# Kernel tuning notes

Hardware: AMD Instinct MI355X
Metric: run time of the kernel (lower is better)

Reference implementation:

```python
import jax, jax.numpy as jnp
import numpy as np

B, S, F, T = 32, 512, 512, 1024  # batch, seq_len(channel dim), feat_dim, time length


def setup_inputs() -> dict:
    key = jax.random.key(0)
    ks = jax.random.split(key, 6)
    scale = 0.05  # keep tanh/softmax in a non-saturated regime
    return {
        "z_robot": jax.random.normal(ks[0], (B, S, T), dtype=jnp.float32),
        "z_human": jax.random.normal(ks[1], (B, S, T), dtype=jnp.float32),
        "W_b": jax.random.normal(ks[2], (S, S), dtype=jnp.float32) * scale,
        "W_q": jax.random.normal(ks[3], (F, S), dtype=jnp.float32) * scale,
        "W_v": jax.random.normal(ks[4], (F, S), dtype=jnp.float32) * scale,
        "w_hq": jax.random.normal(ks[5], (1, F), dtype=jnp.float32) * scale,
    }


def reference(z_robot, z_human, W_b, W_q, W_v, w_hq):
    # aux = W_b @ z_human : [B, S, Th]
    aux = jnp.einsum('su,buh->bsh', W_b, z_human)
    # C = tanh(z_robot^T @ aux) : [B, Tr, Th]
    C = jnp.tanh(jnp.einsum('bst,bsh->bth', z_robot, aux))
    # aux2 = W_v @ z_human : [B, F, Th];  aux3 = W_q @ z_robot : [B, F, Tr]
    aux2 = jnp.einsum('fs,bsh->bfh', W_v, z_human)
    aux3 = jnp.einsum('fs,bst->bft', W_q, z_robot)
    # H_q = tanh(aux3 + aux2 @ C^T) : [B, F, Tr]
    H_q = jnp.tanh(aux3 + jnp.einsum('bfh,bth->bft', aux2, C))
    # a_q = softmax(w_hq @ H_q, axis=2) : [B, 1, Tr]
    a_q = jax.nn.softmax(jnp.einsum('of,bft->bot', w_hq, H_q), axis=2)
    # attn = z_robot @ a_q^T : [B, S, 1]
    attn = jnp.einsum('bst,bot->bso', z_robot, a_q)
    return (attn, a_q, C)
```

## Files before the change

### kernel.cpp

```cpp
#include <hip/hip_runtime.h>
#include <math.h>


using f32x4  = __attribute__((ext_vector_type(4))) float;
using bf16x8 = __attribute__((ext_vector_type(8))) short;

__device__ __forceinline__ ushort f2bf(float x) {
    uint u = __float_as_uint(x);
    return (ushort)((u + 0x7fffu + ((u >> 16) & 1u)) >> 16);
}
__device__ __forceinline__ float bf2f(ushort h) { return __uint_as_float((uint)h << 16); }

__device__ __forceinline__ float fast_tanh(float x) {
    return 1.0f - 2.0f / (__expf(2.0f * x) + 1.0f);
}

__device__ __forceinline__ void gll16(const void* g, void* l) {
    __builtin_amdgcn_global_load_lds(
        (__attribute__((address_space(1))) void*)(void*)g,
        (__attribute__((address_space(3))) void*)l, 16, 0, 0);
}


__global__ __launch_bounds__(256)
void transpose_split_k(const float* __restrict__ in, ushort* __restrict__ hi,
                       ushort* __restrict__ lo, int R, int Cn) {
    __shared__ float tile[32][33];
    const int b = blockIdx.z;
    const float* inb = in + (size_t)b * R * Cn;
    const int c0 = blockIdx.x * 32, r0 = blockIdx.y * 32;
    const int tx = threadIdx.x, ty = threadIdx.y;
    #pragma unroll
    for (int i = 0; i < 32; i += 8)
        tile[ty + i][tx] = inb[(size_t)(r0 + ty + i) * Cn + c0 + tx];
    __syncthreads();
    const size_t ob = (size_t)b * R * Cn;
    #pragma unroll
    for (int i = 0; i < 32; i += 8) {
        const float v = tile[tx][ty + i];
        const ushort h = f2bf(v);
        const size_t o = ob + (size_t)(c0 + ty + i) * R + r0 + tx;
        hi[o] = h;
        lo[o] = f2bf(v - bf2f(h));
    }
}

__global__ __launch_bounds__(256)
void convert_split_k(const float* __restrict__ in, ushort* __restrict__ hi,
                     ushort* __restrict__ lo, int n) {
    const int i = blockIdx.x * 256 + threadIdx.x;
    if (i < n) {
        const float v = in[i];
        const ushort h = f2bf(v);
        hi[i] = h;
        if (lo) lo[i] = f2bf(v - bf2f(h));
    }
}

template <int MODE>
__global__ __launch_bounds__(256)
void gemm_split(const ushort* __restrict__ Ahi, const ushort* __restrict__ Alo,
                long sAb, int ldA,
                const ushort* __restrict__ Bhi, const ushort* __restrict__ Blo,
                long sBb, int ldB, int K,
                ushort* __restrict__ Ohi, ushort* __restrict__ Olo,
                float* __restrict__ Of, ushort* __restrict__ O16,
                int ldO, long sOb) {
    __shared__ __align__(16) ushort lds[16384];
    const int b = blockIdx.z, m0 = blockIdx.y * 128, n0 = blockIdx.x * 128;
    const int t = threadIdx.x, l = t & 63, w = t >> 6, wm = w >> 1, wn = w & 1;

    const int srow = l >> 2;
    const int sch  = ((l & 3) ^ (srow & 3)) * 8;
    const ushort* pAh = Ahi + (long)b * sAb + (long)(m0 + w * 32 + srow) * ldA + sch;
    const ushort* pAl = Alo + (long)b * sAb + (long)(m0 + w * 32 + srow) * ldA + sch;
    const ushort* pBh = Bhi + (long)b * sBb + (long)(n0 + w * 32 + srow) * ldB + sch;
    const ushort* pBl = Blo + (long)b * sBb + (long)(n0 + w * 32 + srow) * ldB + sch;

    const int q = l >> 4;
    int offA[4], offB[4];
    #pragma unroll
    for (int i = 0; i < 4; ++i) {
        const int rA = wm * 64 + i * 16 + (l & 15);
        offA[i] = rA * 32 + (q ^ (rA & 3)) * 8;
        const int rB = wn * 64 + i * 16 + (l & 15);
        offB[i] = rB * 32 + (q ^ (rB & 3)) * 8;
    }

    f32x4 acc[4][4] = {};
    for (int k0 = 0; k0 < K; k0 += 32) {
        #pragma unroll
        for (int tt = 0; tt < 2; ++tt) {
            const int lo_ = (w * 32 + tt * 16) * 32;
            gll16(pAh + (long)(tt * 16) * ldA + k0, lds + lo_);
            gll16(pAl + (long)(tt * 16) * ldA + k0, lds + 4096 + lo_);
            gll16(pBh + (long)(tt * 16) * ldB + k0, lds + 8192 + lo_);
            gll16(pBl + (long)(tt * 16) * ldB + k0, lds + 12288 + lo_);
        }
        __syncthreads();
        bf16x8 ah[4], al4[4], bh[4], bl4[4];
        #pragma unroll
        for (int i = 0; i < 4; ++i) {
            ah[i]  = *(const bf16x8*)&lds[offA[i]];
            al4[i] = *(const bf16x8*)&lds[4096 + offA[i]];
            bh[i]  = *(const bf16x8*)&lds[8192 + offB[i]];
            bl4[i] = *(const bf16x8*)&lds[12288 + offB[i]];
        }
        #pragma unroll
        for (int i = 0; i < 4; ++i)
            #pragma unroll
            for (int j = 0; j < 4; ++j) {
                acc[i][j] = __builtin_amdgcn_mfma_f32_16x16x32_bf16(ah[i],  bh[j],  acc[i][j], 0, 0, 0);
                acc[i][j] = __builtin_amdgcn_mfma_f32_16x16x32_bf16(ah[i],  bl4[j], acc[i][j], 0, 0, 0);
                acc[i][j] = __builtin_amdgcn_mfma_f32_16x16x32_bf16(al4[i], bh[j],  acc[i][j], 0, 0, 0);
            }
        __syncthreads();
    }

    const int cl = l & 15, rl = (l >> 4) * 4;
    #pragma unroll
    for (int i = 0; i < 4; ++i)
        #pragma unroll
        for (int r = 0; r < 4; ++r) {
            const long mg = m0 + wm * 64 + i * 16 + rl + r;
            #pragma unroll
            for (int j = 0; j < 4; ++j) {
                const int ng = n0 + wn * 64 + j * 16 + cl;
                const float v = acc[i][j][r];
                const long o = (long)b * sOb + mg * ldO + ng;
                if (MODE == 0) {
                    const ushort h = f2bf(v);
                    Ohi[o] = h;
                    Olo[o] = f2bf(v - bf2f(h));
                } else {
                    const float tv = fast_tanh(v);
                    Of[o] = tv;
                    O16[o] = f2bf(tv);
                }
            }
        }
}

__device__ __forceinline__ void plain_core(
    const ushort* __restrict__ A, long sAb, int ldA,
    const ushort* __restrict__ B, long sBb, int ldB, int K,
    int b, int m0, int n0, ushort* lds, f32x4 (&acc)[4][4]) {
    const int t = threadIdx.x, l = t & 63, w = t >> 6, wm = w >> 1, wn = w & 1;
    const int srow = l >> 3;
    const int sch  = ((l & 7) ^ (srow & 7)) * 8;
    const ushort* pA = A + (long)b * sAb + (long)(m0 + w * 32 + srow) * ldA + sch;
    const ushort* pB = B + (long)b * sBb + (long)(n0 + w * 32 + srow) * ldB + sch;
    const int q = l >> 4;
    int offA[4], offB[4];
    #pragma unroll
    for (int i = 0; i < 4; ++i) {
        const int rA = wm * 64 + i * 16 + (l & 15);
        offA[i] = rA * 64 + (q ^ (rA & 7)) * 8;
        const int rB = wn * 64 + i * 16 + (l & 15);
        offB[i] = 8192 + rB * 64 + (q ^ (rB & 7)) * 8;
    }
    for (int k0 = 0; k0 < K; k0 += 64) {
        #pragma unroll
        for (int tt = 0; tt < 4; ++tt) {
            gll16(pA + (long)(tt * 8) * ldA + k0, lds + (w * 32 + tt * 8) * 64);
            gll16(pB + (long)(tt * 8) * ldB + k0, lds + 8192 + (w * 32 + tt * 8) * 64);
        }
        __syncthreads();
        #pragma unroll
        for (int s = 0; s < 2; ++s) {
            bf16x8 av[4], bv[4];
            #pragma unroll
            for (int i = 0; i < 4; ++i) {
                av[i] = *(const bf16x8*)&lds[offA[i] ^ (s * 32)];
                bv[i] = *(const bf16x8*)&lds[offB[i] ^ (s * 32)];
            }
            #pragma unroll
            for (int i = 0; i < 4; ++i)
                #pragma unroll
                for (int j = 0; j < 4; ++j)
                    acc[i][j] = __builtin_amdgcn_mfma_f32_16x16x32_bf16(av[i], bv[j], acc[i][j], 0, 0, 0);
        }
        __syncthreads();
    }
}

__global__ __launch_bounds__(256)
void gemm_plain_store(const ushort* __restrict__ A, long sAb, int ldA,
                      const ushort* __restrict__ B, long sBb, int ldB, int K,
                      ushort* __restrict__ O, long sOb, int ldO) {
    __shared__ __align__(16) ushort lds[16384];
    const int b = blockIdx.z, m0 = blockIdx.y * 128, n0 = blockIdx.x * 128;
    f32x4 acc[4][4] = {};
    plain_core(A, sAb, ldA, B, sBb, ldB, K, b, m0, n0, lds, acc);
    const int t = threadIdx.x, l = t & 63, w = t >> 6, wm = w >> 1, wn = w & 1;
    const int cl = l & 15, rl = (l >> 4) * 4;
    #pragma unroll
    for (int i = 0; i < 4; ++i)
        #pragma unroll
        for (int r = 0; r < 4; ++r) {
            const long mg = m0 + wm * 64 + i * 16 + rl + r;
            #pragma unroll
            for (int j = 0; j < 4; ++j)
                O[(long)b * sOb + mg * ldO + n0 + wn * 64 + j * 16 + cl] = f2bf(acc[i][j][r]);
        }
}

__global__ __launch_bounds__(256)
void gemm_fused_logits(const ushort* __restrict__ Wq16, const ushort* __restrict__ zrT,
                       const ushort* __restrict__ aux2, const ushort* __restrict__ C16,
                       const float* __restrict__ whq, float* __restrict__ logits) {
    __shared__ __align__(16) ushort lds[16384];
    const int b = blockIdx.z, m0 = blockIdx.y * 128, n0 = blockIdx.x * 128;
    f32x4 acc[4][4] = {};
    plain_core(Wq16, 0, 512, zrT, 524288, 512, 512, b, m0, n0, lds, acc);
    plain_core(aux2, 524288, 1024, C16, 1048576, 1024, 1024, b, m0, n0, lds, acc);
    const int t = threadIdx.x, l = t & 63, w = t >> 6, wm = w >> 1, wn = w & 1;
    float p[4] = {0.f, 0.f, 0.f, 0.f};
    #pragma unroll
    for (int i = 0; i < 4; ++i)
        #pragma unroll
        for (int r = 0; r < 4; ++r) {
            const float wv = whq[m0 + wm * 64 + i * 16 + (l >> 4) * 4 + r];
            #pragma unroll
            for (int j = 0; j < 4; ++j)
                p[j] += wv * fast_tanh(acc[i][j][r]);
        }
    #pragma unroll
    for (int j = 0; j < 4; ++j) {
        p[j] += __shfl_xor(p[j], 16);
        p[j] += __shfl_xor(p[j], 32);
    }
    float* red = (float*)lds;
    __syncthreads();
    if (l < 16) {
        #pragma unroll
        for (int j = 0; j < 4; ++j)
            red[wm * 128 + wn * 64 + j * 16 + l] = p[j];
    }
    __syncthreads();
    if (t < 128)
        atomicAdd(&logits[(long)b * 1024 + n0 + t], red[t] + red[128 + t]);
}

__global__ __launch_bounds__(256)
void softmax_kernel(const float* __restrict__ logits, float* __restrict__ aq, int T) {
    __shared__ float sm[256];
    const int b = blockIdx.x, tid = threadIdx.x;
    float v[4];
    float mx = -1e30f;
    #pragma unroll
    for (int i = 0; i < 4; ++i) {
        v[i] = logits[(size_t)b * T + tid + 256 * i];
        mx = fmaxf(mx, v[i]);
    }
    sm[tid] = mx; __syncthreads();
    for (int s = 128; s > 0; s >>= 1) {
        if (tid < s) sm[tid] = fmaxf(sm[tid], sm[tid + s]);
        __syncthreads();
    }
    mx = sm[0]; __syncthreads();
    float e[4], sum = 0.f;
    #pragma unroll
    for (int i = 0; i < 4; ++i) { e[i] = __expf(v[i] - mx); sum += e[i]; }
    sm[tid] = sum; __syncthreads();
    for (int s = 128; s > 0; s >>= 1) {
        if (tid < s) sm[tid] += sm[tid + s];
        __syncthreads();
    }
    const float inv = 1.0f / sm[0];
    #pragma unroll
    for (int i = 0; i < 4; ++i)
        aq[(size_t)b * T + tid + 256 * i] = e[i] * inv;
}

__global__ __launch_bounds__(256)
void attn_kernel(const float* __restrict__ ZR, const float* __restrict__ aq,
                 float* __restrict__ out, int S, int T) {
    const int b = blockIdx.y;
    const int s = blockIdx.x * 4 + (threadIdx.x >> 6);
    const int lane = threadIdx.x & 63;
    const float* row = ZR + ((size_t)b * S + s) * T;
    const float* a = aq + (size_t)b * T;
    float sum = 0.f;
    for (int t = lane; t < T; t += 64) sum += row[t] * a[t];
    #pragma unroll
    for (int off = 32; off > 0; off >>= 1) sum += __shfl_down(sum, off, 64);
    if (lane == 0) out[(size_t)b * S + s] = sum;
}

#define BM 64
#define BN 64
#define BK 16
#define PAD 4

__global__ __launch_bounds__(256)
void gemm_nn(const float* __restrict__ A, const float* __restrict__ Bm,
             float* __restrict__ D, int M, int N, int K) {
    __shared__ float As[BK][BM + PAD];
    __shared__ float Bs[BK][BN + PAD];
    const int b = blockIdx.z, m0 = blockIdx.y * BM, n0 = blockIdx.x * BN;
    const int tx = threadIdx.x, ty = threadIdx.y, f = ty * 16 + tx;
    const float* Bb = Bm + (size_t)b * K * N;
    float acc[4][4] = {};
    const int ka = f % 16, ma = f / 16, nb = f % 64, kb = f / 64;
    for (int k0 = 0; k0 < K; k0 += BK) {
        #pragma unroll
        for (int i = 0; i < 4; ++i)
            As[ka][ma + 16 * i] = A[(size_t)(m0 + ma + 16 * i) * K + k0 + ka];
        #pragma unroll
        for (int i = 0; i < 4; ++i)
            Bs[kb + 4 * i][nb] = Bb[(size_t)(k0 + kb + 4 * i) * N + n0 + nb];
        __syncthreads();
        #pragma unroll
        for (int k = 0; k < BK; ++k) {
            float av[4], bv[4];
            *(float4*)av = *(const float4*)&As[k][ty * 4];
            *(float4*)bv = *(const float4*)&Bs[k][tx * 4];
            #pragma unroll
            for (int i = 0; i < 4; ++i)
                #pragma unroll
                for (int j = 0; j < 4; ++j) acc[i][j] += av[i] * bv[j];
        }
        __syncthreads();
    }
    float* Db = D + (size_t)b * M * N;
    #pragma unroll
    for (int i = 0; i < 4; ++i)
        *(float4*)&Db[(size_t)(m0 + ty * 4 + i) * N + n0 + tx * 4] =
            make_float4(acc[i][0], acc[i][1], acc[i][2], acc[i][3]);
}

__global__ __launch_bounds__(256)
void gemm_tn_tanh(const float* __restrict__ ZR, const float* __restrict__ AUX,
                  float* __restrict__ C, int M, int N, int K) {
    __shared__ float As[BK][BM + PAD];
    __shared__ float Bs[BK][BN + PAD];
    const int b = blockIdx.z, m0 = blockIdx.y * BM, n0 = blockIdx.x * BN;
    const int tx = threadIdx.x, ty = threadIdx.y, f = ty * 16 + tx;
    const float* ZRb = ZR + (size_t)b * K * M;
    const float* AUXb = AUX + (size_t)b * K * N;
    float acc[4][4] = {};
    const int nl = f % 64, kl = f / 64;
    for (int k0 = 0; k0 < K; k0 += BK) {
        #pragma unroll
        for (int i = 0; i < 4; ++i)
            As[kl + 4 * i][nl] = ZRb[(size_t)(k0 + kl + 4 * i) * M + m0 + nl];
        #pragma unroll
        for (int i = 0; i < 4; ++i)
            Bs[kl + 4 * i][nl] = AUXb[(size_t)(k0 + kl + 4 * i) * N + n0 + nl];
        __syncthreads();
        #pragma unroll
        for (int k = 0; k < BK; ++k) {
            float av[4], bv[4];
            *(float4*)av = *(const float4*)&As[k][ty * 4];
            *(float4*)bv = *(const float4*)&Bs[k][tx * 4];
            #pragma unroll
            for (int i = 0; i < 4; ++i)
                #pragma unroll
                for (int j = 0; j < 4; ++j) acc[i][j] += av[i] * bv[j];
        }
        __syncthreads();
    }
    float* Cb = C + (size_t)b * M * N;
    #pragma unroll
    for (int i = 0; i < 4; ++i)
        *(float4*)&Cb[(size_t)(m0 + ty * 4 + i) * N + n0 + tx * 4] =
            make_float4(fast_tanh(acc[i][0]), fast_tanh(acc[i][1]),
                        fast_tanh(acc[i][2]), fast_tanh(acc[i][3]));
}

__global__ __launch_bounds__(256)
void gemm_nt_fused(const float* __restrict__ Wq, const float* __restrict__ ZR,
                   const float* __restrict__ A2, const float* __restrict__ Cm,
                   const float* __restrict__ whq, float* __restrict__ logits,
                   int M, int N, int K1, int K2) {
    __shared__ float As[BK][BM + PAD];
    __shared__ float Bs[BK][BN + PAD];
    __shared__ float red[16][BN];
    const int b = blockIdx.z, m0 = blockIdx.y * BM, n0 = blockIdx.x * BN;
    const int tx = threadIdx.x, ty = threadIdx.y, f = ty * 16 + tx;
    const float* ZRb = ZR + (size_t)b * K1 * N;
    const float* A2b = A2 + (size_t)b * M * K2;
    const float* Cb = Cm + (size_t)b * N * K2;
    float acc3[4][4] = {};
    {
        const int ka = f % 16, ma = f / 16, nb = f % 64, kb = f / 64;
        for (int k0 = 0; k0 < K1; k0 += BK) {
            #pragma unroll
            for (int i = 0; i < 4; ++i)
                As[ka][ma + 16 * i] = Wq[(size_t)(m0 + ma + 16 * i) * K1 + k0 + ka];
            #pragma unroll
            for (int i = 0; i < 4; ++i)
                Bs[kb + 4 * i][nb] = ZRb[(size_t)(k0 + kb + 4 * i) * N + n0 + nb];
            __syncthreads();
            #pragma unroll
            for (int k = 0; k < BK; ++k) {
                float av[4], bv[4];
                *(float4*)av = *(const float4*)&As[k][ty * 4];
                *(float4*)bv = *(const float4*)&Bs[k][tx * 4];
                #pragma unroll
                for (int i = 0; i < 4; ++i)
                    #pragma unroll
                    for (int j = 0; j < 4; ++j) acc3[i][j] += av[i] * bv[j];
            }
            __syncthreads();
        }
    }
    float acc[4][4] = {};
    {
        const int ka = f % 16, ra = f / 16;
        for (int k0 = 0; k0 < K2; k0 += BK) {
            #pragma unroll
            for (int i = 0; i < 4; ++i)
                As[ka][ra + 16 * i] = A2b[(size_t)(m0 + ra + 16 * i) * K2 + k0 + ka];
            #pragma unroll
            for (int i = 0; i < 4; ++i)
                Bs[ka][ra + 16 * i] = Cb[(size_t)(n0 + ra + 16 * i) * K2 + k0 + ka];
            __syncthreads();
            #pragma unroll
            for (int k = 0; k < BK; ++k) {
                float av[4], bv[4];
                *(float4*)av = *(const float4*)&As[k][ty * 4];
                *(float4*)bv = *(const float4*)&Bs[k][tx * 4];
                #pragma unroll
                for (int i = 0; i < 4; ++i)
                    #pragma unroll
                    for (int j = 0; j < 4; ++j) acc[i][j] += av[i] * bv[j];
            }
            __syncthreads();
        }
    }
    float p[4] = {0.f, 0.f, 0.f, 0.f};
    #pragma unroll
    for (int i = 0; i < 4; ++i) {
        const float wv = whq[m0 + ty * 4 + i];
        #pragma unroll
        for (int j = 0; j < 4; ++j) p[j] += wv * fast_tanh(acc3[i][j] + acc[i][j]);
    }
    #pragma unroll
    for (int j = 0; j < 4; ++j) red[ty][tx * 4 + j] = p[j];
    __syncthreads();
    if (f < BN) {
        float s = 0.f;
        #pragma unroll
        for (int r = 0; r < 16; ++r) s += red[r][f];
        atomicAdd(&logits[(size_t)b * N + n0 + f], s);
    }
}

extern "C" void kernel_launch(void* const* d_in, const int* in_sizes, int n_in,
                              void* d_out, int out_size, void* d_ws, size_t ws_size,
                              hipStream_t stream) {
    const float* z_robot = (const float*)d_in[0];
    const float* z_human = (const float*)d_in[1];
    const float* W_b     = (const float*)d_in[2];
    const float* W_q     = (const float*)d_in[3];
    const float* W_v     = (const float*)d_in[4];
    const float* w_hq    = (const float*)d_in[5];
    float* out = (float*)d_out;

    const int Bn = 32, S = 512, F = 512, T = 1024;
    float* attn_out = out;
    float* aq_out   = out + (size_t)Bn * S;
    float* C_out    = out + (size_t)Bn * S + (size_t)Bn * T;

    char* ws = (char*)d_ws;
    const size_t E2 = 33554432;

    ushort* zhT_hi  = (ushort*)(ws);
    ushort* zhT_lo  = (ushort*)(ws + E2);
    ushort* zrT_hi  = (ushort*)(ws + 2 * E2);
    ushort* zrT_lo  = (ushort*)(ws + 3 * E2);
    ushort* auxT_hi = (ushort*)(ws + 4 * E2);
    ushort* auxT_lo = (ushort*)(ws + 5 * E2);
    ushort* C16     = (ushort*)(ws + 6 * E2);
    ushort* aux2    = auxT_hi;
    ushort* Wb_hi   = (ushort*)(ws + 8 * E2);
    ushort* Wb_lo   = Wb_hi + 262144;
    ushort* Wq16    = Wb_hi + 524288;
    ushort* Wv16    = Wb_hi + 786432;
    float*  logitsF = (float*)(ws + 8 * E2 + 2097152);
    const size_t FAST_REQ = 8 * E2 + 2097152 + 131072;

    if (ws_size >= FAST_REQ) {
        hipMemsetAsync(logitsF, 0, (size_t)Bn * T * sizeof(float), stream);
        transpose_split_k<<<dim3(32, 16, Bn), dim3(32, 8), 0, stream>>>(z_human, zhT_hi, zhT_lo, 512, 1024);
        transpose_split_k<<<dim3(32, 16, Bn), dim3(32, 8), 0, stream>>>(z_robot, zrT_hi, zrT_lo, 512, 1024);
        convert_split_k<<<dim3(1024), dim3(256), 0, stream>>>(W_b, Wb_hi, Wb_lo, 262144);
        convert_split_k<<<dim3(1024), dim3(256), 0, stream>>>(W_q, Wq16, nullptr, 262144);
        convert_split_k<<<dim3(1024), dim3(256), 0, stream>>>(W_v, Wv16, nullptr, 262144);
        gemm_split<0><<<dim3(4, 8, Bn), dim3(256), 0, stream>>>(
            zhT_hi, zhT_lo, 524288, 512, Wb_hi, Wb_lo, 0, 512, 512,
            auxT_hi, auxT_lo, nullptr, nullptr, 512, 524288);
        gemm_split<1><<<dim3(8, 8, Bn), dim3(256), 0, stream>>>(
            zrT_hi, zrT_lo, 524288, 512, auxT_hi, auxT_lo, 524288, 512, 512,
            nullptr, nullptr, C_out, C16, 1024, 1048576);
        gemm_plain_store<<<dim3(8, 4, Bn), dim3(256), 0, stream>>>(
            Wv16, 0, 512, zhT_hi, 524288, 512, 512, aux2, 524288, 1024);
        gemm_fused_logits<<<dim3(8, 4, Bn), dim3(256), 0, stream>>>(
            Wq16, zrT_hi, aux2, C16, w_hq, logitsF);
        softmax_kernel<<<dim3(Bn), dim3(256), 0, stream>>>(logitsF, aq_out, T);
        attn_kernel<<<dim3(S / 4, Bn), dim3(256), 0, stream>>>(z_robot, aq_out, attn_out, S, T);
    } else {
        float* ws0    = (float*)ws;
        float* logits = (float*)(ws + (size_t)Bn * S * T * 4);
        hipMemsetAsync(logits, 0, (size_t)Bn * T * sizeof(float), stream);
        dim3 blk(16, 16);
        gemm_nn<<<dim3(T / BN, S / BM, Bn), blk, 0, stream>>>(W_b, z_human, ws0, S, T, S);
        gemm_tn_tanh<<<dim3(T / BN, T / BM, Bn), blk, 0, stream>>>(z_robot, ws0, C_out, T, T, S);
        gemm_nn<<<dim3(T / BN, F / BM, Bn), blk, 0, stream>>>(W_v, z_human, ws0, F, T, S);
        gemm_nt_fused<<<dim3(T / BN, F / BM, Bn), blk, 0, stream>>>(
            W_q, z_robot, ws0, C_out, w_hq, logits, F, T, S, T);
        softmax_kernel<<<dim3(Bn), dim3(256), 0, stream>>>(logits, aq_out, T);
        attn_kernel<<<dim3(S / 4, Bn), dim3(256), 0, stream>>>(z_robot, aq_out, attn_out, S, T);
    }
}
```

Measured before the change: 607.3 us.

## Double-buffer LDS tiles in split and plain GEMM cores

Converts the GEMM main loops to a two-stage LDS ping-pong: the next k-tile is issued via global_load_lds into the alternate buffer before computing on the current one, dropping one barrier per iteration. LDS per block doubles to 64 KB and launch bounds request two blocks per SM, which may constrain registers. The trailing barrier moves into plain_core so the logits reduction can reuse LDS safely. Correctness relies on global_load_lds completion being covered by the single barrier (vmcnt wait inserted by the compiler).

```diff
diff --git a/kernel.cpp b/kernel.cpp
--- a/kernel.cpp
+++ b/kernel.cpp
@@ -58,7 +58,7 @@
 }
 
 template <int MODE>
-__global__ __launch_bounds__(256)
+__global__ __launch_bounds__(256, 2)
 void gemm_split(const ushort* __restrict__ Ahi, const ushort* __restrict__ Alo,
                 long sAb, int ldA,
                 const ushort* __restrict__ Bhi, const ushort* __restrict__ Blo,
@@ -66,7 +66,7 @@
                 ushort* __restrict__ Ohi, ushort* __restrict__ Olo,
                 float* __restrict__ Of, ushort* __restrict__ O16,
                 int ldO, long sOb) {
-    __shared__ __align__(16) ushort lds[16384];
+    __shared__ __align__(16) ushort lds[32768];
     const int b = blockIdx.z, m0 = blockIdx.y * 128, n0 = blockIdx.x * 128;
     const int t = threadIdx.x, l = t & 63, w = t >> 6, wm = w >> 1, wn = w & 1;
 
@@ -87,24 +87,32 @@
         offB[i] = rB * 32 + (q ^ (rB & 3)) * 8;
     }
 
-    f32x4 acc[4][4] = {};
-    for (int k0 = 0; k0 < K; k0 += 32) {
+    auto stage = [&](int k0, int st) {
+        const int base = st * 16384;
         #pragma unroll
         for (int tt = 0; tt < 2; ++tt) {
-            const int lo_ = (w * 32 + tt * 16) * 32;
+            const int lo_ = base + (w * 32 + tt * 16) * 32;
             gll16(pAh + (long)(tt * 16) * ldA + k0, lds + lo_);
             gll16(pAl + (long)(tt * 16) * ldA + k0, lds + 4096 + lo_);
             gll16(pBh + (long)(tt * 16) * ldB + k0, lds + 8192 + lo_);
             gll16(pBl + (long)(tt * 16) * ldB + k0, lds + 12288 + lo_);
         }
-        __syncthreads();
+    };
+
+    f32x4 acc[4][4] = {};
+    stage(0, 0);
+    int st = 0;
+    for (int k0 = 0; k0 < K; k0 += 32) {
+        __syncthreads();
+        if (k0 + 32 < K) stage(k0 + 32, st ^ 1);
+        const int base = st * 16384;
         bf16x8 ah[4], al4[4], bh[4], bl4[4];
         #pragma unroll
         for (int i = 0; i < 4; ++i) {
-            ah[i]  = *(const bf16x8*)&lds[offA[i]];
-            al4[i] = *(const bf16x8*)&lds[4096 + offA[i]];
-            bh[i]  = *(const bf16x8*)&lds[8192 + offB[i]];
-            bl4[i] = *(const bf16x8*)&lds[12288 + offB[i]];
+            ah[i]  = *(const bf16x8*)&lds[base + offA[i]];
+            al4[i] = *(const bf16x8*)&lds[base + 4096 + offA[i]];
+            bh[i]  = *(const bf16x8*)&lds[base + 8192 + offB[i]];
+            bl4[i] = *(const bf16x8*)&lds[base + 12288 + offB[i]];
         }
         #pragma unroll
         for (int i = 0; i < 4; ++i)
@@ -114,7 +122,7 @@
                 acc[i][j] = __builtin_amdgcn_mfma_f32_16x16x32_bf16(ah[i],  bl4[j], acc[i][j], 0, 0, 0);
                 acc[i][j] = __builtin_amdgcn_mfma_f32_16x16x32_bf16(al4[i], bh[j],  acc[i][j], 0, 0, 0);
             }
-        __syncthreads();
+        st ^= 1;
     }
 
     const int cl = l & 15, rl = (l >> 4) * 4;
@@ -159,20 +167,27 @@
         const int rB = wn * 64 + i * 16 + (l & 15);
         offB[i] = 8192 + rB * 64 + (q ^ (rB & 7)) * 8;
     }
+    auto stage = [&](int k0, int st) {
+        const int base = st * 16384;
+        #pragma unroll
+        for (int tt = 0; tt < 4; ++tt) {
+            gll16(pA + (long)(tt * 8) * ldA + k0, lds + base + (w * 32 + tt * 8) * 64);
+            gll16(pB + (long)(tt * 8) * ldB + k0, lds + base + 8192 + (w * 32 + tt * 8) * 64);
+        }
+    };
+    stage(0, 0);
+    int st = 0;
     for (int k0 = 0; k0 < K; k0 += 64) {
-        #pragma unroll
-        for (int tt = 0; tt < 4; ++tt) {
-            gll16(pA + (long)(tt * 8) * ldA + k0, lds + (w * 32 + tt * 8) * 64);
-            gll16(pB + (long)(tt * 8) * ldB + k0, lds + 8192 + (w * 32 + tt * 8) * 64);
-        }
-        __syncthreads();
+        __syncthreads();
+        if (k0 + 64 < K) stage(k0 + 64, st ^ 1);
+        const int base = st * 16384;
         #pragma unroll
         for (int s = 0; s < 2; ++s) {
             bf16x8 av[4], bv[4];
             #pragma unroll
             for (int i = 0; i < 4; ++i) {
-                av[i] = *(const bf16x8*)&lds[offA[i] ^ (s * 32)];
-                bv[i] = *(const bf16x8*)&lds[offB[i] ^ (s * 32)];
+                av[i] = *(const bf16x8*)&lds[base + (offA[i] ^ (s * 32))];
+                bv[i] = *(const bf16x8*)&lds[base + (offB[i] ^ (s * 32))];
             }
             #pragma unroll
             for (int i = 0; i < 4; ++i)
@@ -180,15 +195,16 @@
                 for (int j = 0; j < 4; ++j)
                     acc[i][j] = __builtin_amdgcn_mfma_f32_16x16x32_bf16(av[i], bv[j], acc[i][j], 0, 0, 0);
         }
-        __syncthreads();
-    }
-}
-
-__global__ __launch_bounds__(256)
+        st ^= 1;
+    }
+    __syncthreads();
+}
+
+__global__ __launch_bounds__(256, 2)
 void gemm_plain_store(const ushort* __restrict__ A, long sAb, int ldA,
                       const ushort* __restrict__ B, long sBb, int ldB, int K,
                       ushort* __restrict__ O, long sOb, int ldO) {
-    __shared__ __align__(16) ushort lds[16384];
+    __shared__ __align__(16) ushort lds[32768];
     const int b = blockIdx.z, m0 = blockIdx.y * 128, n0 = blockIdx.x * 128;
     f32x4 acc[4][4] = {};
     plain_core(A, sAb, ldA, B, sBb, ldB, K, b, m0, n0, lds, acc);
@@ -205,11 +221,11 @@
         }
 }
 
-__global__ __launch_bounds__(256)
+__global__ __launch_bounds__(256, 2)
 void gemm_fused_logits(const ushort* __restrict__ Wq16, const ushort* __restrict__ zrT,
                        const ushort* __restrict__ aux2, const ushort* __restrict__ C16,
                        const float* __restrict__ whq, float* __restrict__ logits) {
-    __shared__ __align__(16) ushort lds[16384];
+    __shared__ __align__(16) ushort lds[32768];
     const int b = blockIdx.z, m0 = blockIdx.y * 128, n0 = blockIdx.x * 128;
     f32x4 acc[4][4] = {};
     plain_core(Wq16, 0, 512, zrT, 524288, 512, 512, b, m0, n0, lds, acc);
@@ -231,7 +247,6 @@
         p[j] += __shfl_xor(p[j], 32);
     }
     float* red = (float*)lds;
-    __syncthreads();
     if (l < 16) {
         #pragma unroll
         for (int j = 0; j < 4; ++j)
```

After: 580.7 us. -4.4%, faster.
